# Kernel tuning notes

Hardware: AMD Instinct MI355X
Metric: run time of the kernel (lower is better)

## Reference

```python
import jax, jax.numpy as jnp
import numpy as np

N_NODES = 100000
N_EDGES = 3200000


def gcn_conv(x, src, dst, W, b, n):
    # x: [N, Fin] -> linear transform then symmetric-normalized scatter-add (PyG GCNConv)
    xw = x @ W  # [N, Fout]
    loop = jnp.arange(n, dtype=src.dtype)
    s = jnp.concatenate([src, loop])  # add self-loops
    d = jnp.concatenate([dst, loop])
    deg = jax.ops.segment_sum(jnp.ones_like(s, dtype=xw.dtype), d, num_segments=n)
    dinv = jnp.where(deg > 0, jax.lax.rsqrt(deg), 0.0)
    norm = dinv[s] * dinv[d]  # [E+N]
    out = jax.ops.segment_sum(xw[s] * norm[:, None], d, num_segments=n)
    return out + b


def setup_inputs() -> dict:
    key = jax.random.key(0)
    ks = jax.random.split(key, 11)
    x = jax.random.normal(ks[0], (N_NODES, 2), dtype=jnp.float32)
    edge_index = jax.random.randint(ks[1], (2, N_EDGES), 0, N_NODES, dtype=jnp.int64)
    W1 = jax.random.normal(ks[2], (2, 32), dtype=jnp.float32) * 0.5
    b1 = jax.random.normal(ks[3], (32,), dtype=jnp.float32) * 0.1
    W2 = jax.random.normal(ks[4], (32, 32), dtype=jnp.float32) * 0.18
    b2 = jax.random.normal(ks[5], (32,), dtype=jnp.float32) * 0.1
    Wf1 = jax.random.normal(ks[6], (32, 32), dtype=jnp.float32) * 0.18
    bf1 = jax.random.normal(ks[7], (32,), dtype=jnp.float32) * 0.1
    Wf2 = jax.random.normal(ks[8], (32, 1), dtype=jnp.float32) * 0.18
    bf2 = jax.random.normal(ks[9], (1,), dtype=jnp.float32) * 0.1
    return {"x": x, "edge_index": edge_index, "W1": W1, "b1": b1, "W2": W2,
            "b2": b2, "Wf1": Wf1, "bf1": bf1, "Wf2": Wf2, "bf2": bf2}


def reference(x, edge_index, W1, b1, W2, b2, Wf1, bf1, Wf2, bf2):
    n = x.shape[0]
    src, dst = edge_index[0], edge_index[1]
    h = jax.nn.relu(gcn_conv(x, src, dst, W1, b1, n))
    h = jax.nn.relu(gcn_conv(h, src, dst, W2, b2, n))
    h = jax.nn.relu(h @ Wf1 + bf1)
    return h @ Wf2 + bf2  # [N, 1]
```

## Files before the change

### kernel.cpp

```cpp
#include <hip/hip_runtime.h>

#define NGRP 512
#define CAP  6656
#define PTHREADS 1024
#define NE   16
#define EPB  (PTHREADS * NE)
#define SRC_BITS 17
#define SRC_MASK 0x1FFFF

static __device__ __forceinline__ unsigned short f2bf(float f) {
    unsigned u = __float_as_uint(f);
    return (unsigned short)((u + 0x7FFFu + ((u >> 16) & 1u)) >> 16);
}
static __device__ __forceinline__ float bf2f_lo(unsigned u) { return __uint_as_float(u << 16); }
static __device__ __forceinline__ float bf2f_hi(unsigned u) { return __uint_as_float(u & 0xFFFF0000u); }


__global__ __launch_bounds__(PTHREADS) void k_partition(const int* __restrict__ ei, int* gcursor,
                                                        unsigned* __restrict__ pairs,
                                                        int E, int n, int GN) {
    __shared__ int cnt[NGRP];
    __shared__ int cur[NGRP];
    int tid = threadIdx.x;
    if (tid < NGRP) cnt[tid] = 0;
    __syncthreads();
    int base = blockIdx.x * EPB;
    int sreg[NE], dreg[NE];
#pragma unroll
    for (int k = 0; k < NE; ++k) {
        int e = base + tid + k * PTHREADS;
        int d = -1, s = 0;
        if (e < E) {
            s = ei[e];
            d = ei[E + e];
            if ((unsigned)s < (unsigned)n && (unsigned)d < (unsigned)n)
                atomicAdd(&cnt[d / GN], 1);
            else d = -1;
        }
        sreg[k] = s; dreg[k] = d;
    }
    __syncthreads();
    if (tid < NGRP) {
        int c = cnt[tid];
        int rel = c ? atomicAdd(&gcursor[tid], c) : 0;
        cur[tid] = tid * CAP + rel;
    }
    __syncthreads();
#pragma unroll
    for (int k = 0; k < NE; ++k) {
        int d = dreg[k];
        if (d >= 0) {
            int g = d / GN;
            int w = atomicAdd(&cur[g], 1);
            if (w < (g + 1) * CAP)
                pairs[w] = ((unsigned)(d - g * GN) << SRC_BITS) | (unsigned)sreg[k];
        }
    }
}

__global__ __launch_bounds__(512) void k_build(const int* __restrict__ gcursor,
                                               const unsigned* __restrict__ pairs,
                                               const float2* __restrict__ x2,
                                               int* __restrict__ rowStart, int* __restrict__ rowEnd,
                                               int* __restrict__ srclist, float* __restrict__ dinv,
                                               float2* __restrict__ z, int n, int GN) {
    __shared__ unsigned pl[CAP];
    __shared__ int cnt[512];
    __shared__ int cur[512];
    int g = blockIdx.x;
    int t = threadIdx.x;
    int gbeg = g * CAP;
    int m = gcursor[g];
    if (m > CAP) m = CAP;
    cnt[t] = 0;
    __syncthreads();
    for (int k = t; k < m; k += 512) {
        unsigned v = pairs[gbeg + k];
        pl[k] = v;
        atomicAdd(&cnt[(v >> SRC_BITS) & 511], 1);
    }
    __syncthreads();
    int c = cnt[t];
    for (int off = 1; off < 512; off <<= 1) {
        int add = (t >= off) ? cnt[t - off] : 0;
        __syncthreads();
        cnt[t] += add;
        __syncthreads();
    }
    int excl = cnt[t] - c;
    int node = g * GN + t;
    if (t < GN && node < n) {
        int st = gbeg + excl;
        rowStart[node] = st;
        rowEnd[node] = st + c;
        float di = rsqrtf(1.0f + (float)c);
        dinv[node] = di;
        float2 xv = x2[node];
        z[node] = make_float2(xv.x * di, xv.y * di);
    }
    cur[t] = excl;
    __syncthreads();
    for (int k = t; k < m; k += 512) {
        unsigned v = pl[k];
        int dl = (v >> SRC_BITS) & 511;
        int pos = atomicAdd(&cur[dl], 1);
        srclist[gbeg + pos] = (int)(v & SRC_MASK);
    }
}


__global__ __launch_bounds__(256) void k_mid1f(const int* __restrict__ rowStart,
                                               const int* __restrict__ rowEnd,
                                               const int* __restrict__ srclist,
                                               const float2* __restrict__ z,
                                               const float* __restrict__ dinv,
                                               const float* __restrict__ W1,
                                               const float* __restrict__ b1,
                                               const float* __restrict__ W2,
                                               unsigned short* __restrict__ y0,
                                               unsigned short* __restrict__ y1, int n) {
    __shared__ float sW[1024];
    __shared__ float sh[8][33];
    int tid = threadIdx.x;
    for (int k = tid; k < 1024; k += 256) sW[k] = W2[k];
    int ln = tid >> 5, f = tid & 31;
    int i = blockIdx.x * 8 + ln;
    float ax = 0.f, ay = 0.f;
    if (i < n) {
        int e = rowStart[i] + f, end = rowEnd[i];
        for (; e < end; e += 32) {
            float2 v = z[srclist[e]];
            ax += v.x; ay += v.y;
        }
    }
#pragma unroll
    for (int m = 1; m < 32; m <<= 1) {
        ax += __shfl_xor(ax, m, 64);
        ay += __shfl_xor(ay, m, 64);
    }
    float h = 0.f, di = 0.f;
    if (i < n) {
        di = dinv[i];
        float2 zz = z[i];
        ax += zz.x; ay += zz.y;
        h = di * (ax * W1[f] + ay * W1[32 + f]) + b1[f];
        h = h > 0.f ? h : 0.f;
    }
    sh[ln][f] = h;
    __syncthreads();
    if (i < n) {
        float acc = 0.f;
#pragma unroll
        for (int k = 0; k < 32; ++k) acc += sh[ln][k] * sW[k * 32 + f];
        unsigned short* ypl = (f < 16) ? y0 : y1;
        ypl[(size_t)i * 16 + (f & 15)] = f2bf(acc * di);
    }
}

#define ACC8(v)                                        \
    a0 += bf2f_lo((v).x); a1 += bf2f_hi((v).x);        \
    a2 += bf2f_lo((v).y); a3 += bf2f_hi((v).y);        \
    a4 += bf2f_lo((v).z); a5 += bf2f_hi((v).z);        \
    a6 += bf2f_lo((v).w); a7 += bf2f_hi((v).w);

__global__ __launch_bounds__(256) void k_gather_planes(const int* __restrict__ rowStart,
                                                       const int* __restrict__ rowEnd,
                                                       const int* __restrict__ srclist,
                                                       const uint4* __restrict__ yp0,
                                                       const uint4* __restrict__ yp1,
                                                       float4* __restrict__ acc4, int n, int nb) {
    int blk = blockIdx.x;
    int p = (blk >> 2) & 1;
    int b = (blk >> 3) * 4 + (blk & 3);
    if (b >= nb) return;
    const uint4* yh = p ? yp1 : yp0;
    int w = b * 64 + (threadIdx.x >> 2);
    if (w >= n) return;
    int slot = (threadIdx.x >> 1) & 1;
    int q = threadIdx.x & 1;
    int beg = rowStart[w], end = rowEnd[w];
    int deg = end - beg;
    int half = (deg + 1) >> 1;
    int e = beg + slot * half;
    int e1 = slot ? end : (beg + half);
    float a0 = 0.f, a1 = 0.f, a2 = 0.f, a3 = 0.f, a4 = 0.f, a5 = 0.f, a6 = 0.f, a7 = 0.f;
    for (; e + 4 <= e1; e += 4) {
        int s0 = srclist[e], s1 = srclist[e + 1], s2 = srclist[e + 2], s3 = srclist[e + 3];
        uint4 v0 = yh[(size_t)s0 * 2 + q];
        uint4 v1 = yh[(size_t)s1 * 2 + q];
        uint4 v2 = yh[(size_t)s2 * 2 + q];
        uint4 v3 = yh[(size_t)s3 * 2 + q];
        ACC8(v0); ACC8(v1); ACC8(v2); ACC8(v3);
    }
    for (; e < e1; ++e) {
        uint4 v = yh[(size_t)srclist[e] * 2 + q];
        ACC8(v);
    }
    if (slot == 0) {
        uint4 v = yh[(size_t)w * 2 + q];
        ACC8(v);
    }
    a0 += __shfl_xor(a0, 2, 64);
    a1 += __shfl_xor(a1, 2, 64);
    a2 += __shfl_xor(a2, 2, 64);
    a3 += __shfl_xor(a3, 2, 64);
    a4 += __shfl_xor(a4, 2, 64);
    a5 += __shfl_xor(a5, 2, 64);
    a6 += __shfl_xor(a6, 2, 64);
    a7 += __shfl_xor(a7, 2, 64);
    if (slot == 0) {
        float4* dst = acc4 + (size_t)w * 8 + p * 4 + q * 2;
        dst[0] = make_float4(a0, a1, a2, a3);
        dst[1] = make_float4(a4, a5, a6, a7);
    }
}

__global__ void k_final(const float* __restrict__ acc, const float* __restrict__ dinv,
                        const float* __restrict__ b2, const float* __restrict__ Wf1,
                        const float* __restrict__ bf1, const float* __restrict__ Wf2,
                        const float* __restrict__ bf2, float* __restrict__ out, int n) {
    __shared__ float sW[1024];
    __shared__ float sh[8][33];
    int tid = threadIdx.x;
    for (int k = tid; k < 1024; k += 256) sW[k] = Wf1[k];
    int ln = tid >> 5, f = tid & 31;
    int i = blockIdx.x * 8 + ln;
    float h = 0.f;
    if (i < n) {
        h = dinv[i] * acc[(size_t)i * 32 + f] + b2[f];
        h = h > 0.f ? h : 0.f;
    }
    sh[ln][f] = h;
    __syncthreads();
    float p = 0.f;
    if (i < n) {
        float a = bf1[f];
#pragma unroll
        for (int k = 0; k < 32; ++k) a += sh[ln][k] * sW[k * 32 + f];
        a = a > 0.f ? a : 0.f;
        p = a * Wf2[f];
    }
#pragma unroll
    for (int m = 16; m >= 1; m >>= 1) p += __shfl_xor(p, m, 64);
    if (f == 0 && i < n) out[i] = p + bf2[0];
}


extern "C" void kernel_launch(void* const* d_in, const int* in_sizes, int n_in,
                              void* d_out, int out_size, void* d_ws, size_t ws_size,
                              hipStream_t stream) {
    const float* x   = (const float*)d_in[0];
    const int*   ei  = (const int*)d_in[1];
    const float* W1  = (const float*)d_in[2];
    const float* b1  = (const float*)d_in[3];
    const float* W2  = (const float*)d_in[4];
    const float* b2  = (const float*)d_in[5];
    const float* Wf1 = (const float*)d_in[6];
    const float* bf1 = (const float*)d_in[7];
    const float* Wf2 = (const float*)d_in[8];
    const float* bf2 = (const float*)d_in[9];
    float* out = (float*)d_out;

    int n = in_sizes[0] / 2;
    int E = in_sizes[1] / 2;
    int GN = (n + NGRP - 1) / NGRP;

    float* wsf = (float*)d_ws;
    int*    srclist  = (int*)wsf;
    size_t  o = (size_t)NGRP * CAP;
    int*    rowStart = (int*)(wsf + o);     o += n;
    int*    rowEnd   = (int*)(wsf + o);     o += n;
    float*  dinv     = wsf + o;             o += n;
    float2* z        = (float2*)(wsf + o);  o += 2 * (size_t)n;
    int*    gcursor  = (int*)(wsf + o);     o += NGRP;
    o = (o + 3) & ~(size_t)3;
    float*  acc      = wsf + o;             o += 32 * (size_t)n;
    unsigned short* y0 = (unsigned short*)(wsf + o);
    unsigned short* y1 = y0 + (size_t)n * 16;
    unsigned* pairs = (unsigned*)acc;

    int nblk = (E + EPB - 1) / EPB;
    int nb = (n + 63) / 64;
    int nsg = (nb + 3) / 4;

    hipMemsetAsync(gcursor, 0, NGRP * sizeof(int), stream);
    k_partition<<<nblk, PTHREADS, 0, stream>>>(ei, gcursor, pairs, E, n, GN);
    k_build<<<NGRP, 512, 0, stream>>>(gcursor, pairs, (const float2*)x, rowStart, rowEnd,
                                      srclist, dinv, z, n, GN);

    k_mid1f<<<(n + 7) / 8, 256, 0, stream>>>(rowStart, rowEnd, srclist, z, dinv,
                                             W1, b1, W2, y0, y1, n);

    k_gather_planes<<<nsg * 8, 256, 0, stream>>>(rowStart, rowEnd, srclist,
                                                 (const uint4*)y0, (const uint4*)y1,
                                                 (float4*)acc, n, nb);

    k_final<<<(n + 7) / 8, 256, 0, stream>>>(acc, dinv, b2, Wf1, bf1, Wf2, bf2, out, n);
}
```

Measured before the change: 157.3 us.

## Pad CSR rows to multiples of four, vector-load indices, fuse layer-2 epilogue to bf16

Each node's source list is padded to a multiple of four with a dummy index pointing to a zero row appended to z and y. The gather kernel can then read indices as 16-byte vectors with no tail loop. The layer-2 bias, ReLU and normalization move into the gather kernel, which writes bf16 hidden features instead of an fp32 accumulator, so the final MLP kernel reads half as much. Nontemporal loads and stores are added on streaming data, and pairs and srclist get separate buffers. In exchange, padding adds extra gather work on dummy entries and lowers the usable per-group capacity margin, and h2 is rounded to bf16.

After: 180.8 us. 15.0% more time.

```diff
diff --git a/kernel.cpp b/kernel.cpp
--- a/kernel.cpp
+++ b/kernel.cpp
@@ -1,16 +1,19 @@
 #include <hip/hip_runtime.h>
 
 #define NGRP 512
-#define CAP  6656
+#define CAP  7424
 #define PTHREADS 1024
 #define NE   16
 #define EPB  (PTHREADS * NE)
 #define SRC_BITS 17
 #define SRC_MASK 0x1FFFF
 
-static __device__ __forceinline__ unsigned short f2bf(float f) {
+typedef int i4v __attribute__((ext_vector_type(4)));
+typedef unsigned u4v __attribute__((ext_vector_type(4)));
+
+static __device__ __forceinline__ unsigned f2bf(float f) {
     unsigned u = __float_as_uint(f);
-    return (unsigned short)((u + 0x7FFFu + ((u >> 16) & 1u)) >> 16);
+    return (u + 0x7FFFu + ((u >> 16) & 1u)) >> 16;
 }
 static __device__ __forceinline__ float bf2f_lo(unsigned u) { return __uint_as_float(u << 16); }
 static __device__ __forceinline__ float bf2f_hi(unsigned u) { return __uint_as_float(u & 0xFFFF0000u); }
@@ -31,8 +34,8 @@
         int e = base + tid + k * PTHREADS;
         int d = -1, s = 0;
         if (e < E) {
-            s = ei[e];
-            d = ei[E + e];
+            s = __builtin_nontemporal_load(&ei[e]);
+            d = __builtin_nontemporal_load(&ei[E + e]);
             if ((unsigned)s < (unsigned)n && (unsigned)d < (unsigned)n)
                 atomicAdd(&cnt[d / GN], 1);
             else d = -1;
@@ -71,32 +74,39 @@
     int t = threadIdx.x;
     int gbeg = g * CAP;
     int m = gcursor[g];
-    if (m > CAP) m = CAP;
+    const int MCAP = CAP - 600;
+    if (m > MCAP) m = MCAP;
     cnt[t] = 0;
+    if (g == 0 && t == 0) z[n] = make_float2(0.f, 0.f);
     __syncthreads();
     for (int k = t; k < m; k += 512) {
-        unsigned v = pairs[gbeg + k];
+        unsigned v = __builtin_nontemporal_load(&pairs[gbeg + k]);
         pl[k] = v;
         atomicAdd(&cnt[(v >> SRC_BITS) & 511], 1);
     }
     __syncthreads();
     int c = cnt[t];
+    int rnd = (c + 3) & ~3;
+    __syncthreads();
+    cnt[t] = rnd;
+    __syncthreads();
     for (int off = 1; off < 512; off <<= 1) {
         int add = (t >= off) ? cnt[t - off] : 0;
         __syncthreads();
         cnt[t] += add;
         __syncthreads();
     }
-    int excl = cnt[t] - c;
+    int excl = cnt[t] - rnd;
     int node = g * GN + t;
+    int st = gbeg + excl;
     if (t < GN && node < n) {
-        int st = gbeg + excl;
         rowStart[node] = st;
-        rowEnd[node] = st + c;
+        rowEnd[node] = st + rnd;
         float di = rsqrtf(1.0f + (float)c);
         dinv[node] = di;
         float2 xv = x2[node];
         z[node] = make_float2(xv.x * di, xv.y * di);
+        for (int j = c; j < rnd; ++j) srclist[st + j] = n;
     }
     cur[t] = excl;
     __syncthreads();
@@ -129,7 +139,8 @@
     if (i < n) {
         int e = rowStart[i] + f, end = rowEnd[i];
         for (; e < end; e += 32) {
-            float2 v = z[srclist[e]];
+            int s = __builtin_nontemporal_load(&srclist[e]);
+            float2 v = z[s];
             ax += v.x; ay += v.y;
         }
     }
@@ -153,7 +164,10 @@
 #pragma unroll
         for (int k = 0; k < 32; ++k) acc += sh[ln][k] * sW[k * 32 + f];
         unsigned short* ypl = (f < 16) ? y0 : y1;
-        ypl[(size_t)i * 16 + (f & 15)] = f2bf(acc * di);
+        ypl[(size_t)i * 16 + (f & 15)] = (unsigned short)f2bf(acc * di);
+    } else if (i == n) {
+        unsigned short* ypl = (f < 16) ? y0 : y1;
+        ypl[(size_t)n * 16 + (f & 15)] = 0;
     }
 }
 
@@ -168,33 +182,32 @@
                                                        const int* __restrict__ srclist,
                                                        const uint4* __restrict__ yp0,
                                                        const uint4* __restrict__ yp1,
-                                                       float4* __restrict__ acc4, int n, int nb) {
+                                                       const float* __restrict__ dinv,
+                                                       const float* __restrict__ b2,
+                                                       unsigned short* __restrict__ h2_0,
+                                                       unsigned short* __restrict__ h2_1,
+                                                       int n, int nb) {
     int blk = blockIdx.x;
     int p = (blk >> 2) & 1;
     int b = (blk >> 3) * 4 + (blk & 3);
     if (b >= nb) return;
     const uint4* yh = p ? yp1 : yp0;
+    unsigned short* hp = p ? h2_1 : h2_0;
     int w = b * 64 + (threadIdx.x >> 2);
     if (w >= n) return;
     int slot = (threadIdx.x >> 1) & 1;
     int q = threadIdx.x & 1;
-    int beg = rowStart[w], end = rowEnd[w];
-    int deg = end - beg;
-    int half = (deg + 1) >> 1;
-    int e = beg + slot * half;
-    int e1 = slot ? end : (beg + half);
+    int beg = rowStart[w];
+    int nq = (rowEnd[w] - beg) >> 2;
+    const i4v* sl4 = (const i4v*)(srclist + beg);
     float a0 = 0.f, a1 = 0.f, a2 = 0.f, a3 = 0.f, a4 = 0.f, a5 = 0.f, a6 = 0.f, a7 = 0.f;
-    for (; e + 4 <= e1; e += 4) {
-        int s0 = srclist[e], s1 = srclist[e + 1], s2 = srclist[e + 2], s3 = srclist[e + 3];
-        uint4 v0 = yh[(size_t)s0 * 2 + q];
-        uint4 v1 = yh[(size_t)s1 * 2 + q];
-        uint4 v2 = yh[(size_t)s2 * 2 + q];
-        uint4 v3 = yh[(size_t)s3 * 2 + q];
+    for (int j = slot; j < nq; j += 2) {
+        i4v s4 = __builtin_nontemporal_load(&sl4[j]);
+        uint4 v0 = yh[(size_t)s4.x * 2 + q];
+        uint4 v1 = yh[(size_t)s4.y * 2 + q];
+        uint4 v2 = yh[(size_t)s4.z * 2 + q];
+        uint4 v3 = yh[(size_t)s4.w * 2 + q];
         ACC8(v0); ACC8(v1); ACC8(v2); ACC8(v3);
-    }
-    for (; e < e1; ++e) {
-        uint4 v = yh[(size_t)srclist[e] * 2 + q];
-        ACC8(v);
     }
     if (slot == 0) {
         uint4 v = yh[(size_t)w * 2 + q];
@@ -209,16 +222,30 @@
     a6 += __shfl_xor(a6, 2, 64);
     a7 += __shfl_xor(a7, 2, 64);
     if (slot == 0) {
-        float4* dst = acc4 + (size_t)w * 8 + p * 4 + q * 2;
-        dst[0] = make_float4(a0, a1, a2, a3);
-        dst[1] = make_float4(a4, a5, a6, a7);
-    }
-}
-
-__global__ void k_final(const float* __restrict__ acc, const float* __restrict__ dinv,
-                        const float* __restrict__ b2, const float* __restrict__ Wf1,
-                        const float* __restrict__ bf1, const float* __restrict__ Wf2,
-                        const float* __restrict__ bf2, float* __restrict__ out, int n) {
+        float di = dinv[w];
+        const float* bb = b2 + p * 16 + q * 8;
+        float t0 = di * a0 + bb[0]; t0 = t0 > 0.f ? t0 : 0.f;
+        float t1 = di * a1 + bb[1]; t1 = t1 > 0.f ? t1 : 0.f;
+        float t2 = di * a2 + bb[2]; t2 = t2 > 0.f ? t2 : 0.f;
+        float t3 = di * a3 + bb[3]; t3 = t3 > 0.f ? t3 : 0.f;
+        float t4 = di * a4 + bb[4]; t4 = t4 > 0.f ? t4 : 0.f;
+        float t5 = di * a5 + bb[5]; t5 = t5 > 0.f ? t5 : 0.f;
+        float t6 = di * a6 + bb[6]; t6 = t6 > 0.f ? t6 : 0.f;
+        float t7 = di * a7 + bb[7]; t7 = t7 > 0.f ? t7 : 0.f;
+        u4v pk;
+        pk.x = f2bf(t0) | (f2bf(t1) << 16);
+        pk.y = f2bf(t2) | (f2bf(t3) << 16);
+        pk.z = f2bf(t4) | (f2bf(t5) << 16);
+        pk.w = f2bf(t6) | (f2bf(t7) << 16);
+        __builtin_nontemporal_store(pk, (u4v*)(hp + (size_t)w * 16 + q * 8));
+    }
+}
+
+__global__ void k_final(const unsigned short* __restrict__ h2_0,
+                        const unsigned short* __restrict__ h2_1,
+                        const float* __restrict__ Wf1, const float* __restrict__ bf1,
+                        const float* __restrict__ Wf2, const float* __restrict__ bf2,
+                        float* __restrict__ out, int n) {
     __shared__ float sW[1024];
     __shared__ float sh[8][33];
     int tid = threadIdx.x;
@@ -227,8 +254,9 @@
     int i = blockIdx.x * 8 + ln;
     float h = 0.f;
     if (i < n) {
-        h = dinv[i] * acc[(size_t)i * 32 + f] + b2[f];
-        h = h > 0.f ? h : 0.f;
+        const unsigned short* hp = (f < 16) ? h2_0 : h2_1;
+        unsigned short u = __builtin_nontemporal_load(&hp[(size_t)i * 16 + (f & 15)]);
+        h = __uint_as_float((unsigned)u << 16);
     }
     sh[ln][f] = h;
     __syncthreads();
@@ -265,35 +293,39 @@
     int E = in_sizes[1] / 2;
     int GN = (n + NGRP - 1) / NGRP;
 
-    float* wsf = (float*)d_ws;
-    int*    srclist  = (int*)wsf;
-    size_t  o = (size_t)NGRP * CAP;
-    int*    rowStart = (int*)(wsf + o);     o += n;
-    int*    rowEnd   = (int*)(wsf + o);     o += n;
-    float*  dinv     = wsf + o;             o += n;
-    float2* z        = (float2*)(wsf + o);  o += 2 * (size_t)n;
-    int*    gcursor  = (int*)(wsf + o);     o += NGRP;
-    o = (o + 3) & ~(size_t)3;
-    float*  acc      = wsf + o;             o += 32 * (size_t)n;
-    unsigned short* y0 = (unsigned short*)(wsf + o);
-    unsigned short* y1 = y0 + (size_t)n * 16;
-    unsigned* pairs = (unsigned*)acc;
+    char* wp = (char*)d_ws;
+    auto alloc = [&](size_t bytes) {
+        char* ptr = wp;
+        wp += (bytes + 15) & ~(size_t)15;
+        return ptr;
+    };
+    int*      srclist = (int*)     alloc(sizeof(int) * (size_t)NGRP * CAP);
+    unsigned* pairs   = (unsigned*)alloc(sizeof(unsigned) * (size_t)NGRP * CAP);
+    int*      rowStart= (int*)     alloc(sizeof(int) * (size_t)n);
+    int*      rowEnd  = (int*)     alloc(sizeof(int) * (size_t)n);
+    float*    dinv    = (float*)   alloc(sizeof(float) * (size_t)n);
+    float2*   z       = (float2*)  alloc(sizeof(float2) * (size_t)(n + 1));
+    int*      gcursor = (int*)     alloc(sizeof(int) * NGRP);
+    unsigned short* y0  = (unsigned short*)alloc(2 * (size_t)(n + 1) * 16);
+    unsigned short* y1  = (unsigned short*)alloc(2 * (size_t)(n + 1) * 16);
+    unsigned short* h2_0= (unsigned short*)alloc(2 * (size_t)n * 16);
+    unsigned short* h2_1= (unsigned short*)alloc(2 * (size_t)n * 16);
 
     int nblk = (E + EPB - 1) / EPB;
     int nb = (n + 63) / 64;
     int nsg = (nb + 3) / 4;
 
-    hipMemsetAsync(gcursor, 0, NGRP * sizeof(int), stream);
+    (void)hipMemsetAsync(gcursor, 0, NGRP * sizeof(int), stream);
     k_partition<<<nblk, PTHREADS, 0, stream>>>(ei, gcursor, pairs, E, n, GN);
     k_build<<<NGRP, 512, 0, stream>>>(gcursor, pairs, (const float2*)x, rowStart, rowEnd,
                                       srclist, dinv, z, n, GN);
 
-    k_mid1f<<<(n + 7) / 8, 256, 0, stream>>>(rowStart, rowEnd, srclist, z, dinv,
+    k_mid1f<<<(n + 8) / 8, 256, 0, stream>>>(rowStart, rowEnd, srclist, z, dinv,
                                              W1, b1, W2, y0, y1, n);
 
     k_gather_planes<<<nsg * 8, 256, 0, stream>>>(rowStart, rowEnd, srclist,
                                                  (const uint4*)y0, (const uint4*)y1,
-                                                 (float4*)acc, n, nb);
-
-    k_final<<<(n + 7) / 8, 256, 0, stream>>>(acc, dinv, b2, Wf1, bf1, Wf2, bf2, out, n);
-}
+                                                 dinv, b2, h2_0, h2_1, n, nb);
+
+    k_final<<<(n + 7) / 8, 256, 0, stream>>>(h2_0, h2_1, Wf1, bf1, Wf2, bf2, out, n);
+}
```
